# Performance work log

Measured on AMD Instinct MI355X. Metric: run time of the kernel, lower is better.

## Reference

```python
import jax, jax.numpy as jnp
import numpy as np

EPS = 1e-5

def setup_inputs() -> dict:
    key = jax.random.key(0)
    ks = jax.random.split(key, 16)
    B, C, F, T = 8, 32, 32, 4000
    Ch = C // 2  # 16
    inp = {}
    inp["x"] = jax.random.normal(ks[0], (B, C, F, T), dtype=jnp.float32)
    # q/k/v 1x1 conv blocks stacked along leading axis: order [q, k, v]
    inp["qkv_W"] = jax.random.normal(ks[1], (3, Ch, C), dtype=jnp.float32) * 0.1
    inp["qkv_b"] = jax.random.normal(ks[2], (3, Ch), dtype=jnp.float32) * 0.1
    inp["qkv_gamma"] = 1.0 + 0.1 * jax.random.normal(ks[3], (3, Ch), dtype=jnp.float32)
    inp["qkv_beta"] = 0.1 * jax.random.normal(ks[4], (3, Ch), dtype=jnp.float32)
    inp["qkv_mean"] = 0.1 * jax.random.normal(ks[5], (3, Ch), dtype=jnp.float32)
    inp["qkv_var"] = jax.random.uniform(ks[6], (3, Ch), dtype=jnp.float32, minval=0.5, maxval=1.5)
    inp["qkv_alpha"] = jnp.full((3,), 0.25, dtype=jnp.float32)  # PReLU slopes
    # enc 1x1 conv block: Ch -> C
    inp["enc_W"] = jax.random.normal(ks[7], (C, Ch), dtype=jnp.float32) * 0.1
    inp["enc_b"] = jax.random.normal(ks[8], (C,), dtype=jnp.float32) * 0.1
    inp["enc_gamma"] = 1.0 + 0.1 * jax.random.normal(ks[9], (C,), dtype=jnp.float32)
    inp["enc_beta"] = 0.1 * jax.random.normal(ks[10], (C,), dtype=jnp.float32)
    inp["enc_mean"] = 0.1 * jax.random.normal(ks[11], (C,), dtype=jnp.float32)
    inp["enc_var"] = jax.random.uniform(ks[12], (C,), dtype=jnp.float32, minval=0.5, maxval=1.5)
    inp["enc_alpha"] = jnp.asarray(0.25, dtype=jnp.float32)
    return inp


def reference(x, qkv_W, qkv_b, qkv_gamma, qkv_beta, qkv_mean, qkv_var, qkv_alpha,
              enc_W, enc_b, enc_gamma, enc_beta, enc_mean, enc_var, enc_alpha):
    B, C, F, T = x.shape
    Ch = C // 2
    D = Ch * F  # flattened token feature dim
    # --- q/k/v ConvBlocks (1x1 conv + inference BN + PReLU), batched over qkv axis ---
    h = jnp.einsum('noi,bift->nboft', qkv_W, x) + qkv_b[:, None, :, None, None]
    inv = (qkv_gamma / jnp.sqrt(qkv_var + EPS))[:, None, :, None, None]
    h = (h - qkv_mean[:, None, :, None, None]) * inv + qkv_beta[:, None, :, None, None]
    h = jnp.where(h > 0, h, qkv_alpha[:, None, None, None, None] * h)
    q, k, v = h[0], h[1], h[2]  # each [B, Ch, F, T]

    def to_tokens(z):
        return z.reshape(B, D, T).transpose(0, 2, 1)  # [B, T, D]

    scale = float(np.sqrt(D))
    qm = to_tokens(q)
    km = to_tokens(k) / scale
    vm = to_tokens(v)
    # sigmoid-gated attention (no softmax normalization)
    mask = jax.nn.sigmoid(jnp.einsum('btd,bsd->bts', qm, km))  # [B, T, T]
    sa = jnp.einsum('bts,bsd->btd', mask, vm)                   # [B, T, D]
    sa = sa.transpose(0, 2, 1).reshape(B, Ch, F, T)
    # --- enc ConvBlock + residual ---
    e = jnp.einsum('oi,bift->boft', enc_W, sa) + enc_b[None, :, None, None]
    einv = (enc_gamma / jnp.sqrt(enc_var + EPS))[None, :, None, None]
    e = (e - enc_mean[None, :, None, None]) * einv + enc_beta[None, :, None, None]
    e = jnp.where(e > 0, e, enc_alpha * e)
    return e + x
```

## Files before the change

### kernel.cpp

```cpp
#include <hip/hip_runtime.h>

typedef __attribute__((ext_vector_type(8))) short bf16x8;
typedef __attribute__((ext_vector_type(4))) float floatx4;
typedef __attribute__((ext_vector_type(4))) unsigned int uintx4;

#define EPSF 1e-5f
#define RS512 0.04419417382415922f

__device__ __forceinline__ unsigned short f2bf(float f) {
  unsigned int u = __float_as_uint(f);
  u += 0x7fffu + ((u >> 16) & 1u);
  return (unsigned short)(u >> 16);
}

union BFrag { bf16x8 v; int i[4]; unsigned short s[8]; };

__device__ __forceinline__ void gll16(const void* g, void* l) {
  __builtin_amdgcn_global_load_lds(
      (__attribute__((address_space(1))) void*)g,
      (__attribute__((address_space(3))) void*)l, 16, 0, 0);
}

__global__ __launch_bounds__(512) void qkv_kernel(
    const float* __restrict__ x,
    const float* __restrict__ Wq, const float* __restrict__ bq,
    const float* __restrict__ gq, const float* __restrict__ beq,
    const float* __restrict__ mq, const float* __restrict__ vq,
    const float* __restrict__ aq,
    unsigned short* __restrict__ Q, unsigned short* __restrict__ K,
    unsigned short* __restrict__ V) {
  const int b = blockIdx.y;
  const int t0 = blockIdx.x << 4;
  const int tid = threadIdx.x;

  __shared__ unsigned short xs[16 * 1032];
  __shared__ float sW[1536];
  __shared__ float sB[48];
  __shared__ unsigned short vsm[512 * 18];

  for (int idx = tid; idx < 1536; idx += 512) {
    int n = idx >> 9, ch = (idx >> 5) & 15;
    float inv = gq[n * 16 + ch] * rsqrtf(vq[n * 16 + ch] + EPSF);
    if (n == 1) inv *= RS512;
    sW[idx] = Wq[idx] * inv;
  }
  if (tid < 48) {
    int n = tid >> 4;
    float inv = gq[tid] * rsqrtf(vq[tid] + EPSF);
    float bb = (bq[tid] - mq[tid]) * inv + beq[tid];
    if (n == 1) bb *= RS512;
    sB[tid] = bb;
  }
  {
    int tq = tid & 3, rq = tid >> 2;
    const float* xb = x + (size_t)b * 1024 * 4000 + t0 + (tq << 2);
    for (int rr = rq; rr < 1024; rr += 128) {
      float4 f = *(const float4*)(xb + (size_t)rr * 4000);
      xs[(tq * 4 + 0) * 1032 + rr] = f2bf(f.x);
      xs[(tq * 4 + 1) * 1032 + rr] = f2bf(f.y);
      xs[(tq * 4 + 2) * 1032 + rr] = f2bf(f.z);
      xs[(tq * 4 + 3) * 1032 + rr] = f2bf(f.w);
    }
  }
  __syncthreads();

  const int lane = tid & 63, w = tid >> 6;
  const int c = lane & 15, qd = lane >> 4;
  const int wg = w >> 2;
  const int lt = (w & 3) * 4 + qd;
  const int t = t0 + lt;
  const int f0 = (c & 3) * 8;
  const unsigned short* xrow = xs + lt * 1032;
  const float aQ = aq[0], aK = aq[1], aV = aq[2];

  for (int p = 0; p < 2; ++p) {
    const int pp = p + (wg << 1);
    const int ch = (c >> 2) + (pp << 2);
    float acq[8], ack[8], acv[8];
#pragma unroll
    for (int j = 0; j < 8; ++j) {
      acq[j] = sB[ch]; ack[j] = sB[16 + ch]; acv[j] = sB[32 + ch];
    }
    const float* wqp = sW + ch * 32;
    const float* wkp = sW + 512 + ch * 32;
    const float* wvp = sW + 1024 + ch * 32;
    for (int i = 0; i < 32; ++i) {
      BFrag xf;
      xf.v = *(const bf16x8*)(xrow + i * 32 + f0);
      float wqi = wqp[i], wki = wkp[i], wvi2 = wvp[i];
#pragma unroll
      for (int j = 0; j < 8; ++j) {
        float xv = __uint_as_float((unsigned int)xf.s[j] << 16);
        acq[j] += wqi * xv; ack[j] += wki * xv; acv[j] += wvi2 * xv;
      }
    }
    unsigned int qw[4], kw[4];
#pragma unroll
    for (int j2 = 0; j2 < 4; ++j2) {
      float q0 = acq[2 * j2], q1 = acq[2 * j2 + 1];
      q0 = q0 > 0.f ? q0 : aQ * q0; q1 = q1 > 0.f ? q1 : aQ * q1;
      qw[j2] = (unsigned int)f2bf(q0) | ((unsigned int)f2bf(q1) << 16);
      float k0 = ack[2 * j2], k1 = ack[2 * j2 + 1];
      k0 = k0 > 0.f ? k0 : aK * k0; k1 = k1 > 0.f ? k1 : aK * k1;
      kw[j2] = (unsigned int)f2bf(k0) | ((unsigned int)f2bf(k1) << 16);
    }
    const int d0 = (pp << 7) + (c << 3);
    uintx4 qv, kv;
    qv[0] = qw[0]; qv[1] = qw[1]; qv[2] = qw[2]; qv[3] = qw[3];
    kv[0] = kw[0]; kv[1] = kw[1]; kv[2] = kw[2]; kv[3] = kw[3];
    *(uintx4*)(Q + (size_t)(b * 4000 + t) * 512 + d0) = qv;
    *(uintx4*)(K + (size_t)(b * 4000 + t) * 512 + d0) = kv;
#pragma unroll
    for (int j = 0; j < 8; ++j) {
      float v0 = acv[j];
      v0 = v0 > 0.f ? v0 : aV * v0;
      vsm[(d0 + j) * 18 + lt] = f2bf(v0);
    }
  }
  __syncthreads();
  {
    const int st = t0 >> 5;
    const int toff = t0 & 16;
    unsigned short* vt = V + ((size_t)(b * 125 + st) * 512) * 32 + toff;
    for (int i = tid; i < 4096; i += 512) {
      int d = i >> 3, u = i & 7;
      unsigned int w2 = *(unsigned int*)&vsm[d * 18 + 2 * u];
      ((unsigned int*)(vt + d * 32))[u] = w2;
    }
  }
}

__global__ __launch_bounds__(512, 2) void attn_kernel(
    const float* __restrict__ x,
    const float* __restrict__ encW, const float* __restrict__ encb,
    const float* __restrict__ encg, const float* __restrict__ encbe,
    const float* __restrict__ encm, const float* __restrict__ encv,
    const float* __restrict__ enca,
    const unsigned short* __restrict__ Q, const unsigned short* __restrict__ K,
    const unsigned short* __restrict__ V, float* __restrict__ out) {
  const int tid = threadIdx.x;
  const int lane = tid & 63;
  const int w = tid >> 6;
  const int b = blockIdx.x >> 5;
  const int bt0 = (blockIdx.x & 31) << 7;
  const int t0 = bt0 + (w << 4);
  const bool active = t0 < 4000;
  const int c = lane & 15, qd = lane >> 4;

  __shared__ unsigned short Ks[2][32 * 520];
  __shared__ unsigned short Vs[2][512 * 32];

  bf16x8 qf[16];
  {
    const int tq = active ? t0 : 0;
    const unsigned short* qp = Q + (size_t)(b * 4000 + tq + c) * 512 + qd * 8;
#pragma unroll
    for (int ks = 0; ks < 16; ++ks) qf[ks] = *(const bf16x8*)(qp + ks * 32);
  }

  floatx4 acc[32];
#pragma unroll
  for (int md = 0; md < 32; ++md) {
    acc[md][0] = 0.f; acc[md][1] = 0.f; acc[md][2] = 0.f; acc[md][3] = 0.f;
  }

  const unsigned short* Kb = K + (size_t)b * 4000 * 512;
  const unsigned short* Vb = V + (size_t)b * 125 * 16384;
  const int srcA = ((((qd << 1) & 3) << 4) | c) << 2;
  const int srcB = srcA + 64;

  const int r0 = w << 2;
  const int lby = lane * 8;
  const int vmask = ((lane >> 2) & 7) ^ ((lane >> 4) & 1);
  const int vsw = (lane ^ vmask) << 3;

  auto stage = [&](int buf, int it) {
    const unsigned short* kg = Kb + (size_t)it * 32 * 512;
    const unsigned short* vg = Vb + (size_t)it * 16384;
#pragma unroll
    for (int r = 0; r < 4; ++r) {
      gll16(kg + (size_t)(r0 + r) * 512 + lby, &Ks[buf][(r0 + r) * 520]);
      gll16(vg + (size_t)(r0 + r) * 512 + vsw, &Vs[buf][(r0 + r) * 512]);
    }
  };

  stage(0, 0);
  int cur = 0;

#pragma unroll 1
  for (int it = 0; it < 125; ++it) {
    asm volatile("s_waitcnt vmcnt(0)" ::: "memory");
    __syncthreads();
    if (it + 1 < 125) stage(cur ^ 1, it + 1);

    if (active) {
      floatx4 sa0, sa1;
      sa0[0] = sa0[1] = sa0[2] = sa0[3] = 0.f;
      sa1 = sa0;
      const unsigned short* kp = &Ks[cur][c * 520 + qd * 8];
      __builtin_amdgcn_s_setprio(1);
#pragma unroll
      for (int ks = 0; ks < 16; ++ks) {
        bf16x8 k0 = *(const bf16x8*)(kp + ks * 32);
        bf16x8 k1 = *(const bf16x8*)(kp + 16 * 520 + ks * 32);
        sa0 = __builtin_amdgcn_mfma_f32_16x16x32_bf16(k0, qf[ks], sa0, 0, 0, 0);
        sa1 = __builtin_amdgcn_mfma_f32_16x16x32_bf16(k1, qf[ks], sa1, 0, 0, 0);
      }
      __builtin_amdgcn_s_setprio(0);
      float p0 = __builtin_amdgcn_rcpf(1.f + __expf(-sa0[0]));
      float p1 = __builtin_amdgcn_rcpf(1.f + __expf(-sa0[1]));
      float p2 = __builtin_amdgcn_rcpf(1.f + __expf(-sa0[2]));
      float p3 = __builtin_amdgcn_rcpf(1.f + __expf(-sa0[3]));
      float p4 = __builtin_amdgcn_rcpf(1.f + __expf(-sa1[0]));
      float p5 = __builtin_amdgcn_rcpf(1.f + __expf(-sa1[1]));
      float p6 = __builtin_amdgcn_rcpf(1.f + __expf(-sa1[2]));
      float p7 = __builtin_amdgcn_rcpf(1.f + __expf(-sa1[3]));
      int w0 = (int)((unsigned int)f2bf(p0) | ((unsigned int)f2bf(p1) << 16));
      int w1 = (int)((unsigned int)f2bf(p2) | ((unsigned int)f2bf(p3) << 16));
      int w2 = (int)((unsigned int)f2bf(p4) | ((unsigned int)f2bf(p5) << 16));
      int w3 = (int)((unsigned int)f2bf(p6) | ((unsigned int)f2bf(p7) << 16));
      const bool lo = qd < 2;
      int b0a = __builtin_amdgcn_ds_bpermute(srcA, w0);
      int b0b = __builtin_amdgcn_ds_bpermute(srcA, w2);
      int b1a = __builtin_amdgcn_ds_bpermute(srcA, w1);
      int b1b = __builtin_amdgcn_ds_bpermute(srcA, w3);
      int b2a = __builtin_amdgcn_ds_bpermute(srcB, w0);
      int b2b = __builtin_amdgcn_ds_bpermute(srcB, w2);
      int b3a = __builtin_amdgcn_ds_bpermute(srcB, w1);
      int b3b = __builtin_amdgcn_ds_bpermute(srcB, w3);
      BFrag pf;
      pf.i[0] = lo ? b0a : b0b;
      pf.i[1] = lo ? b1a : b1b;
      pf.i[2] = lo ? b2a : b2b;
      pf.i[3] = lo ? b3a : b3b;

      const unsigned short* vp = &Vs[cur][((((c << 2) | qd) ^ (c & 7)) << 3)];
      __builtin_amdgcn_s_setprio(1);
#pragma unroll
      for (int md = 0; md < 32; ++md) {
        bf16x8 vf = *(const bf16x8*)(vp + md * 512);
        acc[md] = __builtin_amdgcn_mfma_f32_16x16x32_bf16(vf, pf.v, acc[md], 0, 0, 0);
      }
      __builtin_amdgcn_s_setprio(0);
    }
    cur ^= 1;
  }

  if (active) {
    const float ealpha = enca[0];
#pragma unroll 1
    for (int o = 0; o < 32; ++o) {
      float inv = encg[o] * rsqrtf(encv[o] + EPSF);
      float bfo = (encb[o] - encm[o]) * inv + encbe[o];
      float wr[16];
#pragma unroll
      for (int i = 0; i < 16; ++i) wr[i] = encW[o * 16 + i];
#pragma unroll
      for (int hi = 0; hi < 2; ++hi) {
#pragma unroll
        for (int rr = 0; rr < 4; ++rr) {
          float e = 0.f;
#pragma unroll
          for (int i = 0; i < 16; ++i) e += wr[i] * acc[2 * i + hi][rr];
          e = e * inv + bfo;
          e = e > 0.f ? e : ealpha * e;
          int fq = (qd << 2) + rr + (hi << 4);
          size_t idx = ((size_t)((b << 5) + o) * 32 + fq) * 4000 + t0 + c;
          out[idx] = e + x[idx];
        }
      }
    }
  }
}

extern "C" void kernel_launch(void* const* d_in, const int* in_sizes, int n_in,
                              void* d_out, int out_size, void* d_ws,
                              size_t ws_size, hipStream_t stream) {
  const float* x = (const float*)d_in[0];
  unsigned short* Q = (unsigned short*)d_ws;
  unsigned short* K = Q + (size_t)8 * 4000 * 512;
  unsigned short* V = K + (size_t)8 * 4000 * 512;

  dim3 g1(250, 8);
  qkv_kernel<<<g1, 512, 0, stream>>>(
      x, (const float*)d_in[1], (const float*)d_in[2], (const float*)d_in[3],
      (const float*)d_in[4], (const float*)d_in[5], (const float*)d_in[6],
      (const float*)d_in[7], Q, K, V);

  attn_kernel<<<dim3(256), 512, 0, stream>>>(
      x, (const float*)d_in[8], (const float*)d_in[9], (const float*)d_in[10],
      (const float*)d_in[11], (const float*)d_in[12], (const float*)d_in[13],
      (const float*)d_in[14], Q, K, V, (float*)d_out);
}
```

Measured before the change: 705.1 us.

## Share sigmoid mask tile via LDS and split PV across waves by D slices

Each wave now writes its bf16 sigmoid probabilities to a shared LDS tile. After a barrier, every wave computes P·V for all 128 query rows of the block, restricted to its own 4 slices of the value dimension. Previously each wave did all 32 D-chunks for its own 16 queries and shuffled P with bpermute. This changes the accumulator layout to 4x8 and lets V fragments be reused across 8 query groups. The cost is an extra block barrier per iteration, plus an LDS round trip to transpose the accumulators back for the enc conv epilogue. Separately, the qkv weight table is padded to stride 33 to avoid LDS bank conflicts.

```diff
diff --git a/kernel.cpp b/kernel.cpp
--- a/kernel.cpp
+++ b/kernel.cpp
@@ -34,7 +34,7 @@
   const int tid = threadIdx.x;
 
   __shared__ unsigned short xs[16 * 1032];
-  __shared__ float sW[1536];
+  __shared__ float sW[1584];
   __shared__ float sB[48];
   __shared__ unsigned short vsm[512 * 18];
 
@@ -42,7 +42,7 @@
     int n = idx >> 9, ch = (idx >> 5) & 15;
     float inv = gq[n * 16 + ch] * rsqrtf(vq[n * 16 + ch] + EPSF);
     if (n == 1) inv *= RS512;
-    sW[idx] = Wq[idx] * inv;
+    sW[n * 528 + ch * 33 + (idx & 31)] = Wq[idx] * inv;
   }
   if (tid < 48) {
     int n = tid >> 4;
@@ -81,9 +81,9 @@
     for (int j = 0; j < 8; ++j) {
       acq[j] = sB[ch]; ack[j] = sB[16 + ch]; acv[j] = sB[32 + ch];
     }
-    const float* wqp = sW + ch * 32;
-    const float* wkp = sW + 512 + ch * 32;
-    const float* wvp = sW + 1024 + ch * 32;
+    const float* wqp = sW + ch * 33;
+    const float* wkp = sW + 528 + ch * 33;
+    const float* wvp = sW + 1056 + ch * 33;
     for (int i = 0; i < 32; ++i) {
       BFrag xf;
       xf.v = *(const bf16x8*)(xrow + i * 32 + f0);
@@ -147,8 +147,13 @@
   const bool active = t0 < 4000;
   const int c = lane & 15, qd = lane >> 4;
 
-  __shared__ unsigned short Ks[2][32 * 520];
-  __shared__ unsigned short Vs[2][512 * 32];
+  __shared__ __align__(16) unsigned char smem[142336];
+  unsigned short* Ksb = (unsigned short*)smem;
+  unsigned short* Vsb = Ksb + 2 * 16640;
+  unsigned short* Pb = Vsb + 2 * 16384;
+  float* Eb = (float*)smem;
+
+  for (int i = tid; i < 2560; i += 512) ((unsigned int*)Pb)[i] = 0u;
 
   bf16x8 qf[16];
   {
@@ -158,16 +163,17 @@
     for (int ks = 0; ks < 16; ++ks) qf[ks] = *(const bf16x8*)(qp + ks * 32);
   }
 
-  floatx4 acc[32];
-#pragma unroll
-  for (int md = 0; md < 32; ++md) {
-    acc[md][0] = 0.f; acc[md][1] = 0.f; acc[md][2] = 0.f; acc[md][3] = 0.f;
-  }
+  floatx4 acc[4][8];
+#pragma unroll
+  for (int m = 0; m < 4; ++m)
+#pragma unroll
+    for (int q2 = 0; q2 < 8; ++q2) {
+      acc[m][q2][0] = 0.f; acc[m][q2][1] = 0.f;
+      acc[m][q2][2] = 0.f; acc[m][q2][3] = 0.f;
+    }
 
   const unsigned short* Kb = K + (size_t)b * 4000 * 512;
   const unsigned short* Vb = V + (size_t)b * 125 * 16384;
-  const int srcA = ((((qd << 1) & 3) << 4) | c) << 2;
-  const int srcB = srcA + 64;
 
   const int r0 = w << 2;
   const int lby = lane * 8;
@@ -175,12 +181,14 @@
   const int vsw = (lane ^ vmask) << 3;
 
   auto stage = [&](int buf, int it) {
-    const unsigned short* kg = Kb + (size_t)it * 32 * 512;
+    const unsigned short* kg = Kb + (size_t)it * 16384;
     const unsigned short* vg = Vb + (size_t)it * 16384;
+    unsigned short* kd = Ksb + buf * 16640;
+    unsigned short* vd = Vsb + buf * 16384;
 #pragma unroll
     for (int r = 0; r < 4; ++r) {
-      gll16(kg + (size_t)(r0 + r) * 512 + lby, &Ks[buf][(r0 + r) * 520]);
-      gll16(vg + (size_t)(r0 + r) * 512 + vsw, &Vs[buf][(r0 + r) * 512]);
+      gll16(kg + (size_t)((r0 + r) << 9) + lby, kd + (r0 + r) * 520);
+      gll16(vg + (size_t)((r0 + r) << 9) + vsw, vd + ((r0 + r) << 9));
     }
   };
 
@@ -197,7 +205,7 @@
       floatx4 sa0, sa1;
       sa0[0] = sa0[1] = sa0[2] = sa0[3] = 0.f;
       sa1 = sa0;
-      const unsigned short* kp = &Ks[cur][c * 520 + qd * 8];
+      const unsigned short* kp = Ksb + cur * 16640 + c * 520 + qd * 8;
       __builtin_amdgcn_s_setprio(1);
 #pragma unroll
       for (int ks = 0; ks < 16; ++ks) {
@@ -215,61 +223,88 @@
       float p5 = __builtin_amdgcn_rcpf(1.f + __expf(-sa1[1]));
       float p6 = __builtin_amdgcn_rcpf(1.f + __expf(-sa1[2]));
       float p7 = __builtin_amdgcn_rcpf(1.f + __expf(-sa1[3]));
-      int w0 = (int)((unsigned int)f2bf(p0) | ((unsigned int)f2bf(p1) << 16));
-      int w1 = (int)((unsigned int)f2bf(p2) | ((unsigned int)f2bf(p3) << 16));
-      int w2 = (int)((unsigned int)f2bf(p4) | ((unsigned int)f2bf(p5) << 16));
-      int w3 = (int)((unsigned int)f2bf(p6) | ((unsigned int)f2bf(p7) << 16));
-      const bool lo = qd < 2;
-      int b0a = __builtin_amdgcn_ds_bpermute(srcA, w0);
-      int b0b = __builtin_amdgcn_ds_bpermute(srcA, w2);
-      int b1a = __builtin_amdgcn_ds_bpermute(srcA, w1);
-      int b1b = __builtin_amdgcn_ds_bpermute(srcA, w3);
-      int b2a = __builtin_amdgcn_ds_bpermute(srcB, w0);
-      int b2b = __builtin_amdgcn_ds_bpermute(srcB, w2);
-      int b3a = __builtin_amdgcn_ds_bpermute(srcB, w1);
-      int b3b = __builtin_amdgcn_ds_bpermute(srcB, w3);
-      BFrag pf;
-      pf.i[0] = lo ? b0a : b0b;
-      pf.i[1] = lo ? b1a : b1b;
-      pf.i[2] = lo ? b2a : b2b;
-      pf.i[3] = lo ? b3a : b3b;
-
-      const unsigned short* vp = &Vs[cur][((((c << 2) | qd) ^ (c & 7)) << 3)];
+      unsigned short* pw = Pb + ((w << 4) + c) * 40 + (qd << 2);
+      uint2 pa, pb2;
+      pa.x = (unsigned int)f2bf(p0) | ((unsigned int)f2bf(p1) << 16);
+      pa.y = (unsigned int)f2bf(p2) | ((unsigned int)f2bf(p3) << 16);
+      pb2.x = (unsigned int)f2bf(p4) | ((unsigned int)f2bf(p5) << 16);
+      pb2.y = (unsigned int)f2bf(p6) | ((unsigned int)f2bf(p7) << 16);
+      *(uint2*)pw = pa;
+      *(uint2*)(pw + 16) = pb2;
+    }
+    __syncthreads();
+
+    {
+      const unsigned short* vp =
+          Vsb + cur * 16384 + ((((c << 2) | qd) ^ (c & 7)) << 3);
+      bf16x8 vf[4];
+#pragma unroll
+      for (int m = 0; m < 4; ++m)
+        vf[m] = *(const bf16x8*)(vp + ((r0 + m) << 9));
       __builtin_amdgcn_s_setprio(1);
 #pragma unroll
-      for (int md = 0; md < 32; ++md) {
-        bf16x8 vf = *(const bf16x8*)(vp + md * 512);
-        acc[md] = __builtin_amdgcn_mfma_f32_16x16x32_bf16(vf, pf.v, acc[md], 0, 0, 0);
+      for (int h = 0; h < 2; ++h) {
+        bf16x8 pf[4];
+#pragma unroll
+        for (int q2 = 0; q2 < 4; ++q2)
+          pf[q2] = *(const bf16x8*)(Pb + ((((h << 2) | q2) << 4) + c) * 40 +
+                                    (qd << 3));
+#pragma unroll
+        for (int m = 0; m < 4; ++m)
+#pragma unroll
+          for (int q2 = 0; q2 < 4; ++q2)
+            acc[m][(h << 2) | q2] = __builtin_amdgcn_mfma_f32_16x16x32_bf16(
+                vf[m], pf[q2], acc[m][(h << 2) | q2], 0, 0, 0);
       }
       __builtin_amdgcn_s_setprio(0);
     }
     cur ^= 1;
   }
 
-  if (active) {
-    const float ealpha = enca[0];
+  __syncthreads();
+
+  const float ealpha = enca[0];
+#pragma unroll
+  for (int rnd = 0; rnd < 2; ++rnd) {
+#pragma unroll
+    for (int m = 0; m < 4; ++m)
+#pragma unroll
+      for (int q2 = 0; q2 < 4; ++q2)
+        *(floatx4*)&Eb[((q2 << 4) + c) * 516 + (w << 6) + (m << 4) +
+                       (qd << 2)] = acc[m][(rnd << 2) | q2];
+    __syncthreads();
+    if ((w >> 2) == rnd && active) {
+      const float* er = Eb + (((w & 3) << 4) + c) * 516;
+#pragma unroll
+      for (int hi = 0; hi < 2; ++hi) {
+        floatx4 sh[16];
+#pragma unroll
+        for (int i = 0; i < 16; ++i)
+          sh[i] = *(const floatx4*)&er[(i << 5) + (hi << 4) + (qd << 2)];
 #pragma unroll 1
-    for (int o = 0; o < 32; ++o) {
-      float inv = encg[o] * rsqrtf(encv[o] + EPSF);
-      float bfo = (encb[o] - encm[o]) * inv + encbe[o];
-      float wr[16];
-#pragma unroll
-      for (int i = 0; i < 16; ++i) wr[i] = encW[o * 16 + i];
-#pragma unroll
-      for (int hi = 0; hi < 2; ++hi) {
-#pragma unroll
-        for (int rr = 0; rr < 4; ++rr) {
-          float e = 0.f;
-#pragma unroll
-          for (int i = 0; i < 16; ++i) e += wr[i] * acc[2 * i + hi][rr];
-          e = e * inv + bfo;
-          e = e > 0.f ? e : ealpha * e;
-          int fq = (qd << 2) + rr + (hi << 4);
-          size_t idx = ((size_t)((b << 5) + o) * 32 + fq) * 4000 + t0 + c;
-          out[idx] = e + x[idx];
+        for (int o = 0; o < 32; ++o) {
+          float inv = encg[o] * rsqrtf(encv[o] + EPSF);
+          float bfo = (encb[o] - encm[o]) * inv + encbe[o];
+          float e0 = 0.f, e1 = 0.f, e2 = 0.f, e3 = 0.f;
+#pragma unroll
+          for (int i = 0; i < 16; ++i) {
+            float wi = encW[(o << 4) + i];
+            e0 += wi * sh[i][0]; e1 += wi * sh[i][1];
+            e2 += wi * sh[i][2]; e3 += wi * sh[i][3];
+          }
+          float ee[4] = {e0, e1, e2, e3};
+#pragma unroll
+          for (int rr = 0; rr < 4; ++rr) {
+            float e = ee[rr] * inv + bfo;
+            e = e > 0.f ? e : ealpha * e;
+            int fq = (qd << 2) + rr + (hi << 4);
+            size_t idx = ((size_t)((b << 5) + o) * 32 + fq) * 4000 + t0 + c;
+            out[idx] = e + x[idx];
+          }
         }
       }
     }
+    __syncthreads();
   }
 }
 
```

Result: faster. 641.0 us (-9.1%).
